# Kernel optimization log

Hardware: AMD Instinct MI355X
Metric: run time of the kernel (lower is better)

The kernel has to match this reference:

```python
import jax, jax.numpy as jnp
import numpy as np

B, N, H, OUT, T = 8192, 82, 10, 5, 3  # batch, n_nodes, hidden, output_channel, time_step


def setup_inputs() -> dict:
    key = jax.random.key(0)
    ks = jax.random.split(key, 20)

    def lin(kw, kb, fin, fout):
        w = jax.random.normal(kw, (fout, fin), jnp.float32) * (1.0 / np.sqrt(fin))
        b = jax.random.normal(kb, (fout,), jnp.float32) * 0.01
        return w, b

    w3w, b3w = lin(ks[0], ks[1], 2 * H, H)
    w3u, b3u = lin(ks[2], ks[3], H, H)
    w4w, b4w = lin(ks[4], ks[5], 2 * H, H)
    w5w, b5w = lin(ks[6], ks[7], 2 * H, H)
    w5u, b5u = lin(ks[8], ks[9], H, H)
    wout, bout = lin(ks[10], ks[11], 2 * H, OUT)
    return {
        'x': jax.random.normal(ks[12], (B, N, H), jnp.float32),
        'in_adj': jax.random.uniform(ks[13], (N, N), jnp.float32),
        'out_adj': jax.random.uniform(ks[14], (N, N), jnp.float32),
        'w3w': w3w, 'b3w': b3w, 'w3u': w3u, 'b3u': b3u,
        'w4w': w4w, 'b4w': b4w, 'w5w': w5w, 'b5w': b5w,
        'w5u': w5u, 'b5u': b5u, 'wout': wout, 'bout': bout,
    }


def _dense(v, w, b):
    return v @ w.T + b


def reference(x, in_adj, out_adj, w3w, b3w, w3u, b3u, w4w, b4w,
              w5w, b5w, w5u, b5u, wout, bout):
    b, n, h = x.shape
    nodes = x  # [B, N, H]
    fn = nodes.reshape(b * n, h)
    for _ in range(T):
        # neighbor aggregation; adjacency shared across batch (torch tiles it with repeat)
        a_in = jnp.einsum('ij,bjh->bih', in_adj, nodes)
        a_out = jnp.einsum('ij,bjh->bih', out_adj, nodes)
        av = jnp.concatenate([a_in, a_out], axis=-1).reshape(b * n, 2 * h)
        fn = nodes.reshape(b * n, h)
        zv = jax.nn.sigmoid(_dense(av, w3w, b3w) + _dense(fn, w3u, b3u))
        # NOTE: original torch code (bug) reuses fc_eq3_u here instead of fc_eq4_u
        rv = jax.nn.sigmoid(_dense(av, w4w, b4w) + _dense(fn, w3u, b3u))
        hv = jnp.tanh(_dense(av, w5w, b5w) + _dense(rv * fn, w5u, b5u))
        fn = (1.0 - zv) * fn + zv * hv
        nodes = fn.reshape(b, n, h)
    out_in = jnp.concatenate([fn, x.reshape(b * n, h)], axis=1)
    output = jnp.tanh(_dense(out_in, wout, bout))
    return output, fn
```

## Files before the change

kernel.cpp:

```cpp
#include <hip/hip_runtime.h>
#include <hip/hip_bf16.h>
#include <math.h>

#define B_TOTAL 8192
#define NN      82
#define HH      10
#define OUTC    5
#define TSTEP   3
#define NB      3
#define THREADS 256
#define KP      96
#define MP      16
#define XS      104

typedef __bf16 bf16x8 __attribute__((ext_vector_type(8)));
typedef float  f32x4  __attribute__((ext_vector_type(4)));

__device__ __forceinline__ float sigmoid_(float x) {
    return 1.0f / (1.0f + __expf(-x));
}
__device__ __forceinline__ float tanh_(float x) {
    float e = __expf(2.0f * x);
    return 1.0f - 2.0f / (e + 1.0f);
}

__global__ void prep_adj_kernel(const float* __restrict__ in_adj,
                                const float* __restrict__ out_adj,
                                __hip_bfloat16* __restrict__ adjP) {
    int idx = blockIdx.x * blockDim.x + threadIdx.x;
    if (idx < 2 * KP * KP) {
        int a   = idx / (KP * KP);
        int rem = idx - a * (KP * KP);
        int i = rem / KP;
        int j = rem - i * KP;
        float v = 0.0f;
        if (i < NN && j < NN) v = (a == 0) ? in_adj[i * NN + j] : out_adj[i * NN + j];
        __hip_bfloat16 hi = __float2bfloat16(v);
        __hip_bfloat16 lo = __float2bfloat16(v - __bfloat162float(hi));
        adjP[idx]               = hi;
        adjP[2 * KP * KP + idx] = lo;
    }
}

__device__ __forceinline__ void gru_update(
    float fn[HH], const float ai[HH], const float ao[HH],
    const float* __restrict__ w3w, const float* __restrict__ b3w,
    const float* __restrict__ w3u, const float* __restrict__ b3u,
    const float* __restrict__ w4w, const float* __restrict__ b4w,
    const float* __restrict__ w5w, const float* __restrict__ b5w,
    const float* __restrict__ w5u, const float* __restrict__ b5u)
{
    float u3[HH];
    #pragma unroll
    for (int h = 0; h < HH; ++h) {
        float s = b3u[h];
        #pragma unroll
        for (int k = 0; k < HH; ++k) s = fmaf(w3u[h * HH + k], fn[k], s);
        u3[h] = s;
    }

    float zv[HH], rv[HH];
    #pragma unroll
    for (int h = 0; h < HH; ++h) {
        float s1 = b3w[h];
        float s2 = b4w[h];
        #pragma unroll
        for (int k = 0; k < HH; ++k) {
            s1 = fmaf(w3w[h * 2 * HH + k],      ai[k], s1);
            s1 = fmaf(w3w[h * 2 * HH + HH + k], ao[k], s1);
            s2 = fmaf(w4w[h * 2 * HH + k],      ai[k], s2);
            s2 = fmaf(w4w[h * 2 * HH + HH + k], ao[k], s2);
        }
        zv[h] = sigmoid_(s1 + u3[h]);
        rv[h] = sigmoid_(s2 + u3[h]);
    }

    float rf[HH];
    #pragma unroll
    for (int k = 0; k < HH; ++k) rf[k] = rv[k] * fn[k];

    #pragma unroll
    for (int h = 0; h < HH; ++h) {
        float s = b5w[h] + b5u[h];
        #pragma unroll
        for (int k = 0; k < HH; ++k) {
            s = fmaf(w5w[h * 2 * HH + k],      ai[k], s);
            s = fmaf(w5w[h * 2 * HH + HH + k], ao[k], s);
            s = fmaf(w5u[h * HH + k],          rf[k], s);
        }
        float hv = tanh_(s);
        fn[h] = fn[h] + zv[h] * (hv - fn[h]);
    }
}

extern "C" __global__ __launch_bounds__(THREADS)
void ggnn_kernel(const float* __restrict__ x,
                 const __hip_bfloat16* __restrict__ adjP,
                 const float* __restrict__ w3w, const float* __restrict__ b3w,
                 const float* __restrict__ w3u, const float* __restrict__ b3u,
                 const float* __restrict__ w4w, const float* __restrict__ b4w,
                 const float* __restrict__ w5w, const float* __restrict__ b5w,
                 const float* __restrict__ w5u, const float* __restrict__ b5u,
                 const float* __restrict__ wout, const float* __restrict__ bout,
                 float* __restrict__ out0, float* __restrict__ out_fn)
{
    __shared__ __align__(16) __hip_bfloat16 XtH[NB * MP][XS];
    __shared__ __align__(16) __hip_bfloat16 XtL[NB * MP][XS];
    __shared__ __align__(16) float uin [NB * NN][12];
    __shared__ __align__(16) float uout[NB * NN][12];

    const int t     = threadIdx.x;
    const int bbase = blockIdx.x * NB;
    const int bl    = t / NN;
    const int node  = t - bl * NN;
    const bool act  = (bl < NB) && (bbase + bl < B_TOTAL);
    const int b     = bbase + bl;

    const int lane = t & 63;
    const int w    = t >> 6;
    const int lo16 = lane & 15;
    const int quad = lane >> 4;

    bf16x8 Bh[3][3], Bl[3][3];
    int ntile_c[3], adj_c[3];
    #pragma unroll
    for (int c = 0; c < 3; ++c) {
        int co = w * 3 + c;
        int nt = co >> 1;
        int ad = co & 1;
        ntile_c[c] = nt;
        adj_c[c]   = ad;
        const __hip_bfloat16* BpH = adjP + ((size_t)ad * KP * KP
                                            + (size_t)(nt * 16 + lo16) * KP
                                            + quad * 8);
        #pragma unroll
        for (int k = 0; k < 3; ++k) {
            Bh[c][k] = *reinterpret_cast<const bf16x8*>(BpH + k * 32);
            Bl[c][k] = *reinterpret_cast<const bf16x8*>(BpH + 2 * KP * KP + k * 32);
        }
    }

    for (int idx = t; idx < NB * NN * HH; idx += THREADS) {
        int b_l = idx / (NN * HH);
        int rem = idx - b_l * (NN * HH);
        int j   = rem / HH;
        int h   = rem - j * HH;
        size_t g = (size_t)bbase * NN * HH + idx;
        float v = (g < (size_t)B_TOTAL * NN * HH) ? x[g] : 0.0f;
        __hip_bfloat16 hi = __float2bfloat16(v);
        __hip_bfloat16 lo = __float2bfloat16(v - __bfloat162float(hi));
        XtH[b_l * MP + h][j] = hi;
        XtL[b_l * MP + h][j] = lo;
    }
    for (int idx = t; idx < NB * MP * (KP - NN); idx += THREADS) {
        int r = idx / (KP - NN);
        int c = idx - r * (KP - NN);
        __hip_bfloat16 z = __float2bfloat16(0.0f);
        XtH[r][NN + c] = z;
        XtL[r][NN + c] = z;
    }

    float fn[HH];
    if (act) {
        const float* xr = x + ((size_t)b * NN + node) * HH;
        #pragma unroll
        for (int h2 = 0; h2 < HH / 2; ++h2) {
            float2 p = reinterpret_cast<const float2*>(xr)[h2];
            fn[2 * h2]     = p.x;
            fn[2 * h2 + 1] = p.y;
        }
    }

    for (int step = 0; step < TSTEP; ++step) {
        __syncthreads();

        #pragma unroll
        for (int mtile = 0; mtile < NB; ++mtile) {
            f32x4 acc[3] = {{0,0,0,0}, {0,0,0,0}, {0,0,0,0}};
            #pragma unroll
            for (int k = 0; k < 3; ++k) {
                bf16x8 ah = *reinterpret_cast<const bf16x8*>(&XtH[mtile * MP + lo16][quad * 8 + k * 32]);
                bf16x8 al = *reinterpret_cast<const bf16x8*>(&XtL[mtile * MP + lo16][quad * 8 + k * 32]);
                #pragma unroll
                for (int c = 0; c < 3; ++c) {
                    acc[c] = __builtin_amdgcn_mfma_f32_16x16x32_bf16(ah, Bh[c][k], acc[c], 0, 0, 0);
                    acc[c] = __builtin_amdgcn_mfma_f32_16x16x32_bf16(al, Bh[c][k], acc[c], 0, 0, 0);
                    acc[c] = __builtin_amdgcn_mfma_f32_16x16x32_bf16(ah, Bl[c][k], acc[c], 0, 0, 0);
                }
            }
            #pragma unroll
            for (int c = 0; c < 3; ++c) {
                int i = ntile_c[c] * 16 + lo16;
                if (i < NN) {
                    float* dst = (adj_c[c] ? &uout[0][0] : &uin[0][0]) + (mtile * NN + i) * 12;
                    if (quad < 2) {
                        *reinterpret_cast<float4*>(dst + quad * 4) =
                            make_float4(acc[c][0], acc[c][1], acc[c][2], acc[c][3]);
                    } else if (quad == 2) {
                        *reinterpret_cast<float2*>(dst + 8) = make_float2(acc[c][0], acc[c][1]);
                    }
                }
            }
        }

        __syncthreads();

        if (act) {
            float ai[HH], ao[HH];
            const float* ui = &uin [bl * NN + node][0];
            const float* uo = &uout[bl * NN + node][0];
            {
                float4 p0 = *reinterpret_cast<const float4*>(ui);
                float4 p1 = *reinterpret_cast<const float4*>(ui + 4);
                float2 p2 = *reinterpret_cast<const float2*>(ui + 8);
                ai[0]=p0.x; ai[1]=p0.y; ai[2]=p0.z; ai[3]=p0.w;
                ai[4]=p1.x; ai[5]=p1.y; ai[6]=p1.z; ai[7]=p1.w;
                ai[8]=p2.x; ai[9]=p2.y;
                float4 q0 = *reinterpret_cast<const float4*>(uo);
                float4 q1 = *reinterpret_cast<const float4*>(uo + 4);
                float2 q2 = *reinterpret_cast<const float2*>(uo + 8);
                ao[0]=q0.x; ao[1]=q0.y; ao[2]=q0.z; ao[3]=q0.w;
                ao[4]=q1.x; ao[5]=q1.y; ao[6]=q1.z; ao[7]=q1.w;
                ao[8]=q2.x; ao[9]=q2.y;
            }
            gru_update(fn, ai, ao, w3w, b3w, w3u, b3u, w4w, b4w, w5w, b5w, w5u, b5u);

            #pragma unroll
            for (int h = 0; h < HH; ++h) {
                __hip_bfloat16 hi = __float2bfloat16(fn[h]);
                __hip_bfloat16 lo = __float2bfloat16(fn[h] - __bfloat162float(hi));
                XtH[bl * MP + h][node] = hi;
                XtL[bl * MP + h][node] = lo;
            }
        }
    }

    if (act) {
        size_t row = (size_t)b * NN + node;
        const float* xr = x + row * HH;
        float xi[HH];
        #pragma unroll
        for (int h2 = 0; h2 < HH / 2; ++h2) {
            float2 p = reinterpret_cast<const float2*>(xr)[h2];
            xi[2 * h2]     = p.x;
            xi[2 * h2 + 1] = p.y;
        }

        #pragma unroll
        for (int c = 0; c < OUTC; ++c) {
            float s = bout[c];
            #pragma unroll
            for (int k = 0; k < HH; ++k) s = fmaf(wout[c * 2 * HH + k],      fn[k], s);
            #pragma unroll
            for (int k = 0; k < HH; ++k) s = fmaf(wout[c * 2 * HH + HH + k], xi[k], s);
            out0[row * OUTC + c] = tanh_(s);
        }
        #pragma unroll
        for (int h2 = 0; h2 < HH / 2; ++h2) {
            reinterpret_cast<float2*>(out_fn + row * HH)[h2] =
                make_float2(fn[2 * h2], fn[2 * h2 + 1]);
        }
    }
}

extern "C" void kernel_launch(void* const* d_in, const int* in_sizes, int n_in,
                              void* d_out, int out_size, void* d_ws, size_t ws_size,
                              hipStream_t stream) {
    const float* x       = (const float*)d_in[0];
    const float* in_adj  = (const float*)d_in[1];
    const float* out_adj = (const float*)d_in[2];
    const float* w3w = (const float*)d_in[3];
    const float* b3w = (const float*)d_in[4];
    const float* w3u = (const float*)d_in[5];
    const float* b3u = (const float*)d_in[6];
    const float* w4w = (const float*)d_in[7];
    const float* b4w = (const float*)d_in[8];
    const float* w5w = (const float*)d_in[9];
    const float* b5w = (const float*)d_in[10];
    const float* w5u = (const float*)d_in[11];
    const float* b5u = (const float*)d_in[12];
    const float* wout = (const float*)d_in[13];
    const float* bout = (const float*)d_in[14];

    __hip_bfloat16* adjP = (__hip_bfloat16*)d_ws;
    float* out0   = (float*)d_out;
    float* out_fn = out0 + (size_t)B_TOTAL * NN * OUTC;

    prep_adj_kernel<<<(2 * KP * KP + 255) / 256, 256, 0, stream>>>(in_adj, out_adj, adjP);

    int grid = (B_TOTAL + NB - 1) / NB;
    ggnn_kernel<<<grid, THREADS, 0, stream>>>(
        x, adjP, w3w, b3w, w3u, b3u, w4w, b4w, w5w, b5w, w5u, b5u,
        wout, bout, out0, out_fn);
}
```

Measured before the change: 268.3 us.

## Move GRU gate linear layers onto MFMA with split-bf16 operands

The per-thread scalar FMA gate projections (W3w/W4w/W5w on aggregated features plus W3u on the hidden state) become a second MFMA GEMM. Weights are packed into register A fragments and features are staged as split hi/lo bf16 rows in shared memory. Blocks shrink to 2 batches on 192 threads with a launch bound of 3 blocks per CU, and adjacency B fragments are reloaded from global each step instead of being held in registers. This cuts VALU work and register pressure, but adds another shared-memory round trip and sync per step, and the gate pre-activations are stored as bf16, which loses precision.

Result: slower. 307.3 us (+14.5%).

```diff
diff --git a/kernel.cpp b/kernel.cpp
--- a/kernel.cpp
+++ b/kernel.cpp
@@ -7,11 +7,16 @@
 #define HH      10
 #define OUTC    5
 #define TSTEP   3
-#define NB      3
-#define THREADS 256
+#define NBB     2
+#define THREADS 192
+#define ROWS    (NBB * NN)
 #define KP      96
 #define MP      16
 #define XS      104
+#define BVS     36
+#define GZS     20
+#define GHS     12
+#define NT_GATE 11
 
 typedef __bf16 bf16x8 __attribute__((ext_vector_type(8)));
 typedef float  f32x4  __attribute__((ext_vector_type(4)));
@@ -22,6 +27,20 @@
 __device__ __forceinline__ float tanh_(float x) {
     float e = __expf(2.0f * x);
     return 1.0f - 2.0f / (e + 1.0f);
+}
+__device__ __forceinline__ unsigned short bfb(__hip_bfloat16 h) {
+    union { __hip_bfloat16 b; unsigned short u; } x; x.b = h; return x.u;
+}
+__device__ __forceinline__ unsigned pack2f(float a, float b) {
+    return (unsigned)bfb(__float2bfloat16(a)) |
+           ((unsigned)bfb(__float2bfloat16(b)) << 16);
+}
+__device__ __forceinline__ __bf16 tobf(float v) {
+    union { __hip_bfloat16 b; __bf16 n; } u; u.b = __float2bfloat16(v); return u.n;
+}
+__device__ __forceinline__ float bfhi(float v) {
+    union { unsigned u; float f; } x;
+    x.u = (unsigned)bfb(__float2bfloat16(v)) << 16; return x.f;
 }
 
 __global__ void prep_adj_kernel(const float* __restrict__ in_adj,
@@ -42,58 +61,7 @@
     }
 }
 
-__device__ __forceinline__ void gru_update(
-    float fn[HH], const float ai[HH], const float ao[HH],
-    const float* __restrict__ w3w, const float* __restrict__ b3w,
-    const float* __restrict__ w3u, const float* __restrict__ b3u,
-    const float* __restrict__ w4w, const float* __restrict__ b4w,
-    const float* __restrict__ w5w, const float* __restrict__ b5w,
-    const float* __restrict__ w5u, const float* __restrict__ b5u)
-{
-    float u3[HH];
-    #pragma unroll
-    for (int h = 0; h < HH; ++h) {
-        float s = b3u[h];
-        #pragma unroll
-        for (int k = 0; k < HH; ++k) s = fmaf(w3u[h * HH + k], fn[k], s);
-        u3[h] = s;
-    }
-
-    float zv[HH], rv[HH];
-    #pragma unroll
-    for (int h = 0; h < HH; ++h) {
-        float s1 = b3w[h];
-        float s2 = b4w[h];
-        #pragma unroll
-        for (int k = 0; k < HH; ++k) {
-            s1 = fmaf(w3w[h * 2 * HH + k],      ai[k], s1);
-            s1 = fmaf(w3w[h * 2 * HH + HH + k], ao[k], s1);
-            s2 = fmaf(w4w[h * 2 * HH + k],      ai[k], s2);
-            s2 = fmaf(w4w[h * 2 * HH + HH + k], ao[k], s2);
-        }
-        zv[h] = sigmoid_(s1 + u3[h]);
-        rv[h] = sigmoid_(s2 + u3[h]);
-    }
-
-    float rf[HH];
-    #pragma unroll
-    for (int k = 0; k < HH; ++k) rf[k] = rv[k] * fn[k];
-
-    #pragma unroll
-    for (int h = 0; h < HH; ++h) {
-        float s = b5w[h] + b5u[h];
-        #pragma unroll
-        for (int k = 0; k < HH; ++k) {
-            s = fmaf(w5w[h * 2 * HH + k],      ai[k], s);
-            s = fmaf(w5w[h * 2 * HH + HH + k], ao[k], s);
-            s = fmaf(w5u[h * HH + k],          rf[k], s);
-        }
-        float hv = tanh_(s);
-        fn[h] = fn[h] + zv[h] * (hv - fn[h]);
-    }
-}
-
-extern "C" __global__ __launch_bounds__(THREADS)
+extern "C" __global__ __launch_bounds__(THREADS, 3)
 void ggnn_kernel(const float* __restrict__ x,
                  const __hip_bfloat16* __restrict__ adjP,
                  const float* __restrict__ w3w, const float* __restrict__ b3w,
@@ -104,16 +72,18 @@
                  const float* __restrict__ wout, const float* __restrict__ bout,
                  float* __restrict__ out0, float* __restrict__ out_fn)
 {
-    __shared__ __align__(16) __hip_bfloat16 XtH[NB * MP][XS];
-    __shared__ __align__(16) __hip_bfloat16 XtL[NB * MP][XS];
-    __shared__ __align__(16) float uin [NB * NN][12];
-    __shared__ __align__(16) float uout[NB * NN][12];
+    __shared__ __align__(16) __hip_bfloat16 XtH[NBB * MP][XS];
+    __shared__ __align__(16) __hip_bfloat16 XtL[NBB * MP][XS];
+    __shared__ __align__(16) __hip_bfloat16 BvH[176][BVS];
+    __shared__ __align__(16) __hip_bfloat16 BvL[176][BVS];
+    __shared__ __align__(16) __hip_bfloat16 Gz[ROWS][GZS];
+    __shared__ __align__(16) float          Gh[ROWS][GHS];
 
     const int t     = threadIdx.x;
-    const int bbase = blockIdx.x * NB;
+    const int bbase = blockIdx.x * NBB;
     const int bl    = t / NN;
     const int node  = t - bl * NN;
-    const bool act  = (bl < NB) && (bbase + bl < B_TOTAL);
+    const bool act  = (t < ROWS);
     const int b     = bbase + bl;
 
     const int lane = t & 63;
@@ -121,43 +91,54 @@
     const int lo16 = lane & 15;
     const int quad = lane >> 4;
 
-    bf16x8 Bh[3][3], Bl[3][3];
-    int ntile_c[3], adj_c[3];
+    bf16x8 WAh[2], WAl[2];
     #pragma unroll
-    for (int c = 0; c < 3; ++c) {
-        int co = w * 3 + c;
-        int nt = co >> 1;
-        int ad = co & 1;
-        ntile_c[c] = nt;
-        adj_c[c]   = ad;
-        const __hip_bfloat16* BpH = adjP + ((size_t)ad * KP * KP
-                                            + (size_t)(nt * 16 + lo16) * KP
-                                            + quad * 8);
-        #pragma unroll
-        for (int k = 0; k < 3; ++k) {
-            Bh[c][k] = *reinterpret_cast<const bf16x8*>(BpH + k * 32);
-            Bl[c][k] = *reinterpret_cast<const bf16x8*>(BpH + 2 * KP * KP + k * 32);
-        }
-    }
-
-    for (int idx = t; idx < NB * NN * HH; idx += THREADS) {
-        int b_l = idx / (NN * HH);
-        int rem = idx - b_l * (NN * HH);
-        int j   = rem / HH;
-        int h   = rem - j * HH;
-        size_t g = (size_t)bbase * NN * HH + idx;
-        float v = (g < (size_t)B_TOTAL * NN * HH) ? x[g] : 0.0f;
+    for (int mt = 0; mt < 2; ++mt) {
+        int m = mt * 16 + lo16;
+        #pragma unroll
+        for (int j = 0; j < 8; ++j) {
+            int k = quad * 8 + j;
+            float wv = 0.0f;
+            if (m < 30 && k < 30) {
+                if (k < 20) {
+                    if (m < 10)      wv = w3w[m * 20 + k];
+                    else if (m < 20) wv = w4w[(m - 10) * 20 + k];
+                    else             wv = w5w[(m - 20) * 20 + k];
+                } else {
+                    int ku = k - 20;
+                    if (m < 10)      wv = w3u[m * 10 + ku];
+                    else if (m < 20) wv = w3u[(m - 10) * 10 + ku];
+                }
+            }
+            float hi = bfhi(wv);
+            WAh[mt][j] = tobf(wv);
+            WAl[mt][j] = tobf(wv - hi);
+        }
+    }
+
+    for (int idx = t; idx < NBB * HH * KP; idx += THREADS) {
+        int b_l = idx / (HH * KP);
+        int rem = idx - b_l * (HH * KP);
+        int h   = rem / KP;
+        int j   = rem - h * KP;
+        float v = 0.0f;
+        if (j < NN) v = x[((size_t)(bbase + b_l) * NN + j) * HH + h];
         __hip_bfloat16 hi = __float2bfloat16(v);
         __hip_bfloat16 lo = __float2bfloat16(v - __bfloat162float(hi));
         XtH[b_l * MP + h][j] = hi;
         XtL[b_l * MP + h][j] = lo;
-    }
-    for (int idx = t; idx < NB * MP * (KP - NN); idx += THREADS) {
-        int r = idx / (KP - NN);
-        int c = idx - r * (KP - NN);
-        __hip_bfloat16 z = __float2bfloat16(0.0f);
-        XtH[r][NN + c] = z;
-        XtL[r][NN + c] = z;
+        if (j < NN) {
+            BvH[b_l * NN + j][20 + h] = hi;
+            BvL[b_l * NN + j][20 + h] = lo;
+        }
+    }
+    for (int r = t; r < ROWS; r += THREADS) {
+        *reinterpret_cast<unsigned*>(&BvH[r][30]) = 0u;
+        *reinterpret_cast<unsigned*>(&BvL[r][30]) = 0u;
+        *reinterpret_cast<unsigned*>(&BvH[r][32]) = 0u;
+        *reinterpret_cast<unsigned*>(&BvL[r][32]) = 0u;
+        *reinterpret_cast<unsigned*>(&BvH[r][34]) = 0u;
+        *reinterpret_cast<unsigned*>(&BvL[r][34]) = 0u;
     }
 
     float fn[HH];
@@ -170,61 +151,140 @@
             fn[2 * h2 + 1] = p.y;
         }
     }
+    __syncthreads();
 
     for (int step = 0; step < TSTEP; ++step) {
+        {
+            bf16x8 AH[2][3], AL[2][3];
+            #pragma unroll
+            for (int mt = 0; mt < 2; ++mt)
+                #pragma unroll
+                for (int k = 0; k < 3; ++k) {
+                    AH[mt][k] = *reinterpret_cast<const bf16x8*>(&XtH[mt * MP + lo16][quad * 8 + k * 32]);
+                    AL[mt][k] = *reinterpret_cast<const bf16x8*>(&XtL[mt * MP + lo16][quad * 8 + k * 32]);
+                }
+            #pragma unroll
+            for (int c = 0; c < 4; ++c) {
+                int combo = w * 4 + c;
+                int nt = combo >> 1;
+                int ad = combo & 1;
+                const __hip_bfloat16* base = adjP + (size_t)ad * KP * KP
+                                           + (size_t)(nt * 16 + lo16) * KP + quad * 8;
+                bf16x8 Bh[3], Bl[3];
+                #pragma unroll
+                for (int k = 0; k < 3; ++k) {
+                    Bh[k] = *reinterpret_cast<const bf16x8*>(base + k * 32);
+                    Bl[k] = *reinterpret_cast<const bf16x8*>(base + 2 * KP * KP + k * 32);
+                }
+                #pragma unroll
+                for (int mt = 0; mt < 2; ++mt) {
+                    f32x4 acc = {0.0f, 0.0f, 0.0f, 0.0f};
+                    #pragma unroll
+                    for (int k = 0; k < 3; ++k) {
+                        acc = __builtin_amdgcn_mfma_f32_16x16x32_bf16(AH[mt][k], Bh[k], acc, 0, 0, 0);
+                        acc = __builtin_amdgcn_mfma_f32_16x16x32_bf16(AL[mt][k], Bh[k], acc, 0, 0, 0);
+                        acc = __builtin_amdgcn_mfma_f32_16x16x32_bf16(AH[mt][k], Bl[k], acc, 0, 0, 0);
+                    }
+                    int i = nt * 16 + lo16;
+                    if (i < NN) {
+                        int rr = mt * NN + i;
+                        int kb = ad * 10 + quad * 4;
+                        if (quad < 2) {
+                            *reinterpret_cast<unsigned*>(&BvH[rr][kb])     = pack2f(acc[0], acc[1]);
+                            *reinterpret_cast<unsigned*>(&BvH[rr][kb + 2]) = pack2f(acc[2], acc[3]);
+                            float l0 = acc[0] - bfhi(acc[0]), l1 = acc[1] - bfhi(acc[1]);
+                            float l2 = acc[2] - bfhi(acc[2]), l3 = acc[3] - bfhi(acc[3]);
+                            *reinterpret_cast<unsigned*>(&BvL[rr][kb])     = pack2f(l0, l1);
+                            *reinterpret_cast<unsigned*>(&BvL[rr][kb + 2]) = pack2f(l2, l3);
+                        } else if (quad == 2) {
+                            *reinterpret_cast<unsigned*>(&BvH[rr][kb]) = pack2f(acc[0], acc[1]);
+                            float l0 = acc[0] - bfhi(acc[0]), l1 = acc[1] - bfhi(acc[1]);
+                            *reinterpret_cast<unsigned*>(&BvL[rr][kb]) = pack2f(l0, l1);
+                        }
+                    }
+                }
+            }
+        }
         __syncthreads();
 
-        #pragma unroll
-        for (int mtile = 0; mtile < NB; ++mtile) {
-            f32x4 acc[3] = {{0,0,0,0}, {0,0,0,0}, {0,0,0,0}};
-            #pragma unroll
-            for (int k = 0; k < 3; ++k) {
-                bf16x8 ah = *reinterpret_cast<const bf16x8*>(&XtH[mtile * MP + lo16][quad * 8 + k * 32]);
-                bf16x8 al = *reinterpret_cast<const bf16x8*>(&XtL[mtile * MP + lo16][quad * 8 + k * 32]);
-                #pragma unroll
-                for (int c = 0; c < 3; ++c) {
-                    acc[c] = __builtin_amdgcn_mfma_f32_16x16x32_bf16(ah, Bh[c][k], acc[c], 0, 0, 0);
-                    acc[c] = __builtin_amdgcn_mfma_f32_16x16x32_bf16(al, Bh[c][k], acc[c], 0, 0, 0);
-                    acc[c] = __builtin_amdgcn_mfma_f32_16x16x32_bf16(ah, Bl[c][k], acc[c], 0, 0, 0);
-                }
-            }
-            #pragma unroll
-            for (int c = 0; c < 3; ++c) {
-                int i = ntile_c[c] * 16 + lo16;
-                if (i < NN) {
-                    float* dst = (adj_c[c] ? &uout[0][0] : &uin[0][0]) + (mtile * NN + i) * 12;
-                    if (quad < 2) {
-                        *reinterpret_cast<float4*>(dst + quad * 4) =
-                            make_float4(acc[c][0], acc[c][1], acc[c][2], acc[c][3]);
-                    } else if (quad == 2) {
-                        *reinterpret_cast<float2*>(dst + 8) = make_float2(acc[c][0], acc[c][1]);
+        {
+            int t0 = w * 4;
+            int t1 = (t0 + 4 < NT_GATE) ? t0 + 4 : NT_GATE;
+            for (int tile = t0; tile < t1; ++tile) {
+                int row = tile * 16 + lo16;
+                uint2 h0 = *reinterpret_cast<const uint2*>(&BvH[row][quad * 8]);
+                uint2 h1 = *reinterpret_cast<const uint2*>(&BvH[row][quad * 8 + 4]);
+                uint2 l0 = *reinterpret_cast<const uint2*>(&BvL[row][quad * 8]);
+                uint2 l1 = *reinterpret_cast<const uint2*>(&BvL[row][quad * 8 + 4]);
+                union { uint4 q; bf16x8 v; } bh, bll;
+                bh.q  = make_uint4(h0.x, h0.y, h1.x, h1.y);
+                bll.q = make_uint4(l0.x, l0.y, l1.x, l1.y);
+                #pragma unroll
+                for (int mt = 0; mt < 2; ++mt) {
+                    f32x4 acc = {0.0f, 0.0f, 0.0f, 0.0f};
+                    acc = __builtin_amdgcn_mfma_f32_16x16x32_bf16(WAh[mt], bh.v,  acc, 0, 0, 0);
+                    acc = __builtin_amdgcn_mfma_f32_16x16x32_bf16(WAl[mt], bh.v,  acc, 0, 0, 0);
+                    acc = __builtin_amdgcn_mfma_f32_16x16x32_bf16(WAh[mt], bll.v, acc, 0, 0, 0);
+                    if (row < ROWS) {
+                        if (mt == 0) {
+                            uint2 pk;
+                            pk.x = pack2f(acc[0], acc[1]);
+                            pk.y = pack2f(acc[2], acc[3]);
+                            *reinterpret_cast<uint2*>(&Gz[row][quad * 4]) = pk;
+                        } else {
+                            if (quad == 0) {
+                                uint2 pk;
+                                pk.x = pack2f(acc[0], acc[1]);
+                                pk.y = pack2f(acc[2], acc[3]);
+                                *reinterpret_cast<uint2*>(&Gz[row][16]) = pk;
+                            } else {
+                                *reinterpret_cast<float4*>(&Gh[row][quad * 4 - 4]) =
+                                    make_float4(acc[0], acc[1], acc[2], acc[3]);
+                            }
+                        }
                     }
                 }
             }
         }
-
         __syncthreads();
 
         if (act) {
-            float ai[HH], ao[HH];
-            const float* ui = &uin [bl * NN + node][0];
-            const float* uo = &uout[bl * NN + node][0];
+            float g[20];
+            const uint2* gz = reinterpret_cast<const uint2*>(&Gz[t][0]);
+            #pragma unroll
+            for (int p = 0; p < 5; ++p) {
+                uint2 u = gz[p];
+                g[4 * p + 0] = __uint_as_float(u.x << 16);
+                g[4 * p + 1] = __uint_as_float(u.x & 0xffff0000u);
+                g[4 * p + 2] = __uint_as_float(u.y << 16);
+                g[4 * p + 3] = __uint_as_float(u.y & 0xffff0000u);
+            }
+            float hp[HH];
             {
-                float4 p0 = *reinterpret_cast<const float4*>(ui);
-                float4 p1 = *reinterpret_cast<const float4*>(ui + 4);
-                float2 p2 = *reinterpret_cast<const float2*>(ui + 8);
-                ai[0]=p0.x; ai[1]=p0.y; ai[2]=p0.z; ai[3]=p0.w;
-                ai[4]=p1.x; ai[5]=p1.y; ai[6]=p1.z; ai[7]=p1.w;
-                ai[8]=p2.x; ai[9]=p2.y;
-                float4 q0 = *reinterpret_cast<const float4*>(uo);
-                float4 q1 = *reinterpret_cast<const float4*>(uo + 4);
-                float2 q2 = *reinterpret_cast<const float2*>(uo + 8);
-                ao[0]=q0.x; ao[1]=q0.y; ao[2]=q0.z; ao[3]=q0.w;
-                ao[4]=q1.x; ao[5]=q1.y; ao[6]=q1.z; ao[7]=q1.w;
-                ao[8]=q2.x; ao[9]=q2.y;
-            }
-            gru_update(fn, ai, ao, w3w, b3w, w3u, b3u, w4w, b4w, w5w, b5w, w5u, b5u);
-
+                float4 a = *reinterpret_cast<const float4*>(&Gh[t][0]);
+                float4 c = *reinterpret_cast<const float4*>(&Gh[t][4]);
+                float2 d = *reinterpret_cast<const float2*>(&Gh[t][8]);
+                hp[0]=a.x; hp[1]=a.y; hp[2]=a.z; hp[3]=a.w;
+                hp[4]=c.x; hp[5]=c.y; hp[6]=c.z; hp[7]=c.w;
+                hp[8]=d.x; hp[9]=d.y;
+            }
+            float zv[HH], rf[HH];
+            #pragma unroll
+            for (int h = 0; h < HH; ++h)
+                zv[h] = sigmoid_(g[h] + b3w[h] + b3u[h]);
+            #pragma unroll
+            for (int h = 0; h < HH; ++h) {
+                float rv = sigmoid_(g[10 + h] + b4w[h] + b3u[h]);
+                rf[h] = rv * fn[h];
+            }
+            #pragma unroll
+            for (int h = 0; h < HH; ++h) {
+                float s = hp[h] + b5w[h] + b5u[h];
+                #pragma unroll
+                for (int k = 0; k < HH; ++k) s = fmaf(w5u[h * HH + k], rf[k], s);
+                float hv = tanh_(s);
+                fn[h] = fn[h] + zv[h] * (hv - fn[h]);
+            }
             #pragma unroll
             for (int h = 0; h < HH; ++h) {
                 __hip_bfloat16 hi = __float2bfloat16(fn[h]);
@@ -232,7 +292,15 @@
                 XtH[bl * MP + h][node] = hi;
                 XtL[bl * MP + h][node] = lo;
             }
-        }
+            #pragma unroll
+            for (int p = 0; p < 5; ++p) {
+                float v0 = fn[2 * p], v1 = fn[2 * p + 1];
+                *reinterpret_cast<unsigned*>(&BvH[t][20 + 2 * p]) = pack2f(v0, v1);
+                float l0 = v0 - bfhi(v0), l1 = v1 - bfhi(v1);
+                *reinterpret_cast<unsigned*>(&BvL[t][20 + 2 * p]) = pack2f(l0, l1);
+            }
+        }
+        __syncthreads();
     }
 
     if (act) {
@@ -245,7 +313,6 @@
             xi[2 * h2]     = p.x;
             xi[2 * h2 + 1] = p.y;
         }
-
         #pragma unroll
         for (int c = 0; c < OUTC; ++c) {
             float s = bout[c];
@@ -288,8 +355,7 @@
 
     prep_adj_kernel<<<(2 * KP * KP + 255) / 256, 256, 0, stream>>>(in_adj, out_adj, adjP);
 
-    int grid = (B_TOTAL + NB - 1) / NB;
-    ggnn_kernel<<<grid, THREADS, 0, stream>>>(
+    ggnn_kernel<<<B_TOTAL / NBB, THREADS, 0, stream>>>(
         x, adjP, w3w, b3w, w3u, b3u, w4w, b4w, w5w, b5w, w5u, b5u,
         wout, bout, out0, out_fn);
 }
```

## Transpose aggregation buffers and use packed FMA for GRU update

Applied to the files above, without the earlier changes.

Stores the MFMA aggregation results in transposed per-hidden-channel planes indexed by thread, so each thread reads its inputs with conflict-free scalar LDS loads instead of strided 12-float rows. Rewrites the GRU gate math with two-wide vector FMAs (packed fp32 FMA) and paired weight loads, splitting each dot product into two partial sums. Adds a min-waves hint of 4 to launch bounds, which may constrain registers. Summation order changes slightly, which can shift rounding.

Measured after the change: 227.6 us. -15.2%, faster.

```diff
diff --git a/kernel.cpp b/kernel.cpp
--- a/kernel.cpp
+++ b/kernel.cpp
@@ -12,9 +12,11 @@
 #define KP      96
 #define MP      16
 #define XS      104
+#define UTS     248
 
 typedef __bf16 bf16x8 __attribute__((ext_vector_type(8)));
 typedef float  f32x4  __attribute__((ext_vector_type(4)));
+typedef float  f32x2  __attribute__((ext_vector_type(2)));
 
 __device__ __forceinline__ float sigmoid_(float x) {
     return 1.0f / (1.0f + __expf(-x));
@@ -22,6 +24,12 @@
 __device__ __forceinline__ float tanh_(float x) {
     float e = __expf(2.0f * x);
     return 1.0f - 2.0f / (e + 1.0f);
+}
+__device__ __forceinline__ f32x2 ld2(const float* p) {
+    return *reinterpret_cast<const f32x2*>(p);
+}
+__device__ __forceinline__ f32x2 fma2(f32x2 a, f32x2 b, f32x2 c) {
+    return __builtin_elementwise_fma(a, b, c);
 }
 
 __global__ void prep_adj_kernel(const float* __restrict__ in_adj,
@@ -42,58 +50,7 @@
     }
 }
 
-__device__ __forceinline__ void gru_update(
-    float fn[HH], const float ai[HH], const float ao[HH],
-    const float* __restrict__ w3w, const float* __restrict__ b3w,
-    const float* __restrict__ w3u, const float* __restrict__ b3u,
-    const float* __restrict__ w4w, const float* __restrict__ b4w,
-    const float* __restrict__ w5w, const float* __restrict__ b5w,
-    const float* __restrict__ w5u, const float* __restrict__ b5u)
-{
-    float u3[HH];
-    #pragma unroll
-    for (int h = 0; h < HH; ++h) {
-        float s = b3u[h];
-        #pragma unroll
-        for (int k = 0; k < HH; ++k) s = fmaf(w3u[h * HH + k], fn[k], s);
-        u3[h] = s;
-    }
-
-    float zv[HH], rv[HH];
-    #pragma unroll
-    for (int h = 0; h < HH; ++h) {
-        float s1 = b3w[h];
-        float s2 = b4w[h];
-        #pragma unroll
-        for (int k = 0; k < HH; ++k) {
-            s1 = fmaf(w3w[h * 2 * HH + k],      ai[k], s1);
-            s1 = fmaf(w3w[h * 2 * HH + HH + k], ao[k], s1);
-            s2 = fmaf(w4w[h * 2 * HH + k],      ai[k], s2);
-            s2 = fmaf(w4w[h * 2 * HH + HH + k], ao[k], s2);
-        }
-        zv[h] = sigmoid_(s1 + u3[h]);
-        rv[h] = sigmoid_(s2 + u3[h]);
-    }
-
-    float rf[HH];
-    #pragma unroll
-    for (int k = 0; k < HH; ++k) rf[k] = rv[k] * fn[k];
-
-    #pragma unroll
-    for (int h = 0; h < HH; ++h) {
-        float s = b5w[h] + b5u[h];
-        #pragma unroll
-        for (int k = 0; k < HH; ++k) {
-            s = fmaf(w5w[h * 2 * HH + k],      ai[k], s);
-            s = fmaf(w5w[h * 2 * HH + HH + k], ao[k], s);
-            s = fmaf(w5u[h * HH + k],          rf[k], s);
-        }
-        float hv = tanh_(s);
-        fn[h] = fn[h] + zv[h] * (hv - fn[h]);
-    }
-}
-
-extern "C" __global__ __launch_bounds__(THREADS)
+extern "C" __global__ __launch_bounds__(THREADS, 4)
 void ggnn_kernel(const float* __restrict__ x,
                  const __hip_bfloat16* __restrict__ adjP,
                  const float* __restrict__ w3w, const float* __restrict__ b3w,
@@ -106,8 +63,8 @@
 {
     __shared__ __align__(16) __hip_bfloat16 XtH[NB * MP][XS];
     __shared__ __align__(16) __hip_bfloat16 XtL[NB * MP][XS];
-    __shared__ __align__(16) float uin [NB * NN][12];
-    __shared__ __align__(16) float uout[NB * NN][12];
+    __shared__ float uinT [HH][UTS];
+    __shared__ float uoutT[HH][UTS];
 
     const int t     = threadIdx.x;
     const int bbase = blockIdx.x * NB;
@@ -160,14 +117,13 @@
         XtL[r][NN + c] = z;
     }
 
-    float fn[HH];
+    f32x2 fn2[5];
     if (act) {
         const float* xr = x + ((size_t)b * NN + node) * HH;
         #pragma unroll
-        for (int h2 = 0; h2 < HH / 2; ++h2) {
-            float2 p = reinterpret_cast<const float2*>(xr)[h2];
-            fn[2 * h2]     = p.x;
-            fn[2 * h2 + 1] = p.y;
+        for (int p = 0; p < 5; ++p) {
+            float2 v = reinterpret_cast<const float2*>(xr)[p];
+            fn2[p].x = v.x; fn2[p].y = v.y;
         }
     }
 
@@ -192,12 +148,15 @@
             for (int c = 0; c < 3; ++c) {
                 int i = ntile_c[c] * 16 + lo16;
                 if (i < NN) {
-                    float* dst = (adj_c[c] ? &uout[0][0] : &uin[0][0]) + (mtile * NN + i) * 12;
+                    int col = mtile * NN + i;
+                    float* plane0 = adj_c[c] ? &uoutT[0][0] : &uinT[0][0];
                     if (quad < 2) {
-                        *reinterpret_cast<float4*>(dst + quad * 4) =
-                            make_float4(acc[c][0], acc[c][1], acc[c][2], acc[c][3]);
+                        #pragma unroll
+                        for (int r = 0; r < 4; ++r)
+                            plane0[(quad * 4 + r) * UTS + col] = acc[c][r];
                     } else if (quad == 2) {
-                        *reinterpret_cast<float2*>(dst + 8) = make_float2(acc[c][0], acc[c][1]);
+                        plane0[8 * UTS + col] = acc[c][0];
+                        plane0[9 * UTS + col] = acc[c][1];
                     }
                 }
             }
@@ -206,29 +165,61 @@
         __syncthreads();
 
         if (act) {
-            float ai[HH], ao[HH];
-            const float* ui = &uin [bl * NN + node][0];
-            const float* uo = &uout[bl * NN + node][0];
-            {
-                float4 p0 = *reinterpret_cast<const float4*>(ui);
-                float4 p1 = *reinterpret_cast<const float4*>(ui + 4);
-                float2 p2 = *reinterpret_cast<const float2*>(ui + 8);
-                ai[0]=p0.x; ai[1]=p0.y; ai[2]=p0.z; ai[3]=p0.w;
-                ai[4]=p1.x; ai[5]=p1.y; ai[6]=p1.z; ai[7]=p1.w;
-                ai[8]=p2.x; ai[9]=p2.y;
-                float4 q0 = *reinterpret_cast<const float4*>(uo);
-                float4 q1 = *reinterpret_cast<const float4*>(uo + 4);
-                float2 q2 = *reinterpret_cast<const float2*>(uo + 8);
-                ao[0]=q0.x; ao[1]=q0.y; ao[2]=q0.z; ao[3]=q0.w;
-                ao[4]=q1.x; ao[5]=q1.y; ao[6]=q1.z; ao[7]=q1.w;
-                ao[8]=q2.x; ao[9]=q2.y;
-            }
-            gru_update(fn, ai, ao, w3w, b3w, w3u, b3u, w4w, b4w, w5w, b5w, w5u, b5u);
-
-            #pragma unroll
-            for (int h = 0; h < HH; ++h) {
-                __hip_bfloat16 hi = __float2bfloat16(fn[h]);
-                __hip_bfloat16 lo = __float2bfloat16(fn[h] - __bfloat162float(hi));
+            f32x2 av2[10];
+            #pragma unroll
+            for (int p = 0; p < 5; ++p) {
+                av2[p].x     = uinT [2 * p][t];
+                av2[p].y     = uinT [2 * p + 1][t];
+                av2[5 + p].x = uoutT[2 * p][t];
+                av2[5 + p].y = uoutT[2 * p + 1][t];
+            }
+
+            float u3[HH];
+            #pragma unroll
+            for (int h = 0; h < HH; ++h) {
+                f32x2 s2 = {0.0f, 0.0f};
+                #pragma unroll
+                for (int p = 0; p < 5; ++p)
+                    s2 = fma2(ld2(w3u + h * HH + 2 * p), fn2[p], s2);
+                u3[h] = b3u[h] + s2.x + s2.y;
+            }
+
+            float zv[HH];
+            f32x2 rf2[5];
+            #pragma unroll
+            for (int h = 0; h < HH; ++h) {
+                f32x2 z2 = {0.0f, 0.0f}, r2 = {0.0f, 0.0f};
+                #pragma unroll
+                for (int p = 0; p < 10; ++p) {
+                    z2 = fma2(ld2(w3w + h * 20 + 2 * p), av2[p], z2);
+                    r2 = fma2(ld2(w4w + h * 20 + 2 * p), av2[p], r2);
+                }
+                zv[h] = sigmoid_(b3w[h] + z2.x + z2.y + u3[h]);
+                float rv = sigmoid_(b4w[h] + r2.x + r2.y + u3[h]);
+                float fnh = (h & 1) ? fn2[h >> 1].y : fn2[h >> 1].x;
+                if (h & 1) rf2[h >> 1].y = rv * fnh; else rf2[h >> 1].x = rv * fnh;
+            }
+
+            #pragma unroll
+            for (int h = 0; h < HH; ++h) {
+                f32x2 s2 = {0.0f, 0.0f};
+                #pragma unroll
+                for (int p = 0; p < 10; ++p)
+                    s2 = fma2(ld2(w5w + h * 20 + 2 * p), av2[p], s2);
+                #pragma unroll
+                for (int p = 0; p < 5; ++p)
+                    s2 = fma2(ld2(w5u + h * HH + 2 * p), rf2[p], s2);
+                float hv = tanh_(b5w[h] + b5u[h] + s2.x + s2.y);
+                float fnh = (h & 1) ? fn2[h >> 1].y : fn2[h >> 1].x;
+                fnh = fnh + zv[h] * (hv - fnh);
+                if (h & 1) fn2[h >> 1].y = fnh; else fn2[h >> 1].x = fnh;
+            }
+
+            #pragma unroll
+            for (int h = 0; h < HH; ++h) {
+                float fnh = (h & 1) ? fn2[h >> 1].y : fn2[h >> 1].x;
+                __hip_bfloat16 hi = __float2bfloat16(fnh);
+                __hip_bfloat16 lo = __float2bfloat16(fnh - __bfloat162float(hi));
                 XtH[bl * MP + h][node] = hi;
                 XtL[bl * MP + h][node] = lo;
             }
@@ -238,27 +229,27 @@
     if (act) {
         size_t row = (size_t)b * NN + node;
         const float* xr = x + row * HH;
-        float xi[HH];
-        #pragma unroll
-        for (int h2 = 0; h2 < HH / 2; ++h2) {
-            float2 p = reinterpret_cast<const float2*>(xr)[h2];
-            xi[2 * h2]     = p.x;
-            xi[2 * h2 + 1] = p.y;
+        f32x2 xi2[5];
+        #pragma unroll
+        for (int p = 0; p < 5; ++p) {
+            float2 v = reinterpret_cast<const float2*>(xr)[p];
+            xi2[p].x = v.x; xi2[p].y = v.y;
         }
 
         #pragma unroll
         for (int c = 0; c < OUTC; ++c) {
-            float s = bout[c];
-            #pragma unroll
-            for (int k = 0; k < HH; ++k) s = fmaf(wout[c * 2 * HH + k],      fn[k], s);
-            #pragma unroll
-            for (int k = 0; k < HH; ++k) s = fmaf(wout[c * 2 * HH + HH + k], xi[k], s);
-            out0[row * OUTC + c] = tanh_(s);
-        }
-        #pragma unroll
-        for (int h2 = 0; h2 < HH / 2; ++h2) {
-            reinterpret_cast<float2*>(out_fn + row * HH)[h2] =
-                make_float2(fn[2 * h2], fn[2 * h2 + 1]);
+            f32x2 s2 = {0.0f, 0.0f};
+            #pragma unroll
+            for (int p = 0; p < 5; ++p) {
+                s2 = fma2(ld2(wout + c * 20 + 2 * p),      fn2[p], s2);
+                s2 = fma2(ld2(wout + c * 20 + 10 + 2 * p), xi2[p], s2);
+            }
+            out0[row * OUTC + c] = tanh_(bout[c] + s2.x + s2.y);
+        }
+        #pragma unroll
+        for (int p = 0; p < 5; ++p) {
+            reinterpret_cast<float2*>(out_fn + row * HH)[p] =
+                make_float2(fn2[p].x, fn2[p].y);
         }
     }
 }
```
